# Optimization experiments

Hardware: AMD Instinct MI355X
Metric: run time of the kernel (lower is better)

## Reference

```python
import jax, jax.numpy as jnp
import numpy as np

CLS_W = 1.0
REG_W = 1.0
POS_THR = 0.6
THR_LOW = 0.3
THR_HIGH = 0.6
N_POS = 16
N_NEG = 48
BATCH = 4096
NUM_ANCHOR = 5
FS = 17
SEARCH = 255


def make_anchors():
    # SiamRPN-style anchors: 5 aspect ratios, base size 64, stride 8, 17x17 grid
    ratios = np.array([0.33, 0.5, 1.0, 2.0, 3.0], dtype=np.float64)
    size, stride = 64.0, 8
    ws = np.sqrt(size * size / ratios)            # (K,)
    hs = ws * ratios                              # (K,)
    c = (np.arange(FS) - FS // 2) * stride + SEARCH // 2  # grid centers
    cx = np.broadcast_to(c[None, None, :], (NUM_ANCHOR, FS, FS))
    cy = np.broadcast_to(c[None, :, None], (NUM_ANCHOR, FS, FS))
    w = np.broadcast_to(ws[:, None, None], (NUM_ANCHOR, FS, FS))
    h = np.broadcast_to(hs[:, None, None], (NUM_ANCHOR, FS, FS))
    center = np.stack([cx, cy, w, h], 0).reshape(4, -1).T               # (A,4) cx,cy,w,h
    corner = np.stack([cx - w / 2, cy - h / 2, cx + w / 2, cy + h / 2], 0).reshape(4, -1).T
    return center.astype(np.float32), corner.astype(np.float32)


def setup_inputs() -> dict:
    key = jax.random.key(0)
    k1, k2, k3, k4 = jax.random.split(key, 4)
    pred_cls = jax.random.normal(k1, (BATCH, NUM_ANCHOR, FS, FS), dtype=jnp.float32)
    pred_reg = jax.random.normal(k2, (BATCH, 4, NUM_ANCHOR, FS, FS), dtype=jnp.float32)
    # valid GT boxes inside the search region, overlapping anchor sizes
    cxy = jax.random.uniform(k3, (BATCH, 2), minval=90.0, maxval=165.0)
    wh = jax.random.uniform(k4, (BATCH, 2), minval=35.0, maxval=110.0)
    gt_bbox = jnp.concatenate([cxy - wh / 2, cxy + wh / 2], axis=1).astype(jnp.float32)
    center, corner = make_anchors()
    return {
        "pred_cls": pred_cls,
        "pred_reg": pred_reg,
        "gt_bbox": gt_bbox,
        "anchor_center": jnp.asarray(center),
        "anchor_corner": jnp.asarray(corner),
    }


def jaccard(box_a, box_b):
    # box_a (N,4), box_b (A,4) in x1,y1,x2,y2 -> (N,A) IoU
    lt = jnp.maximum(box_a[:, None, :2], box_b[None, :, :2])
    rb = jnp.minimum(box_a[:, None, 2:], box_b[None, :, 2:])
    wh = jnp.clip(rb - lt, 0.0)
    inter = wh[..., 0] * wh[..., 1]
    area_a = (box_a[:, 2] - box_a[:, 0]) * (box_a[:, 3] - box_a[:, 1])
    area_b = (box_b[:, 2] - box_b[:, 0]) * (box_b[:, 3] - box_b[:, 1])
    return inter / (area_a[:, None] + area_b[None, :] - inter)


def _rand_rank(k, m, A):
    # rank of each index among masked entries under a random shuffle
    u = jax.random.uniform(k, (A,))
    s = jnp.where(m, u, jnp.inf)
    order = jnp.argsort(s)
    return jnp.zeros((A,), jnp.int32).at[order].set(jnp.arange(A, dtype=jnp.int32))


def _forward(pred_cls, pred_reg, gt_bbox, anchor_center, anchor_corner):
    N = pred_cls.shape[0]
    A = anchor_center.shape[0]
    iou = jaccard(gt_bbox, anchor_corner)                       # (N,A)
    matched = jnp.where(iou > THR_HIGH, 1.0, jnp.where(iou < THR_LOW, 0.0, -1.0))
    ks = jax.random.split(jax.random.key(42), 2 * N)
    kpos, kneg = ks[:N], ks[N:]

    def per_sample(cls, reg, gt, mask, kp, kn):
        clsf = cls.reshape(-1)                                  # (A,)
        regf = reg.reshape(4, -1).T                             # (A,4)
        pos = mask == 1.0
        neg = mask == 0.0
        n_pos = jnp.sum(pos).astype(jnp.int32)
        n_neg = jnp.sum(neg).astype(jnp.int32)
        rp = _rand_rank(kp, pos, A)
        rn = _rand_rank(kn, neg, A)
        k_p = jnp.minimum(n_pos, N_POS)                         # sampled positives
        k_n_cap = jnp.where(n_pos > 0, 3 * n_pos, N_NEG)        # int(n_pos*48/16) = 3*n_pos
        k_n = jnp.minimum(n_neg, k_n_cap)
        sel_p = pos & (rp < k_p)
        sel_n = neg & (rn < k_n)
        bce_p = jnp.logaddexp(0.0, -clsf)                       # BCEWithLogits, target 1
        bce_n = jnp.logaddexp(0.0, clsf)                        # BCEWithLogits, target 0
        denom = jnp.maximum(k_p + k_n, 1).astype(clsf.dtype)
        loss_cls_i = (jnp.sum(bce_p * sel_p) + jnp.sum(bce_n * sel_n)) / denom
        acc_i = (jnp.sum((clsf >= POS_THR) & pos) + jnp.sum((clsf < POS_THR) & (~pos))).astype(clsf.dtype) / A
        gcx = (gt[0] + gt[2]) * 0.5
        gcy = (gt[1] + gt[3]) * 0.5
        gw = gt[2] - gt[0]
        gh = gt[3] - gt[1]
        acx, acy, aw, ah = anchor_center[:, 0], anchor_center[:, 1], anchor_center[:, 2], anchor_center[:, 3]
        tgt = jnp.stack([(gcx - acx) / aw, (gcy - acy) / ah, jnp.log(gw / aw), jnp.log(gh / ah)], axis=1)
        np_safe = jnp.maximum(n_pos, 1).astype(clsf.dtype)
        loss_reg_i = jnp.where(n_pos > 0,
                               jnp.sum(((regf - tgt) ** 2) * pos[:, None]) / (4.0 * np_safe),
                               0.0)
        return loss_cls_i, loss_reg_i, acc_i

    lc, lr, ac = jax.vmap(per_sample)(pred_cls, pred_reg, gt_bbox, matched, kpos, kneg)
    loss_cls = jnp.mean(lc)
    loss_reg = jnp.mean(lr)
    acc_cls = jnp.mean(ac)
    loss_total = CLS_W * loss_cls + REG_W * loss_reg
    return loss_total, loss_cls, loss_reg, acc_cls


def reference(pred_cls, pred_reg, gt_bbox, anchor_center, anchor_corner):
    return _forward(pred_cls, pred_reg, gt_bbox, anchor_center, anchor_corner)
```

## Files before the change

### kernel.cpp

```cpp
#include <hip/hip_runtime.h>
#include <stdint.h>
#include <math.h>


#define A_TOT 1445
#define NITER 23
#define WPB 4
#define POS_MAX 64
#define CAND_MAX 128

__device__ __forceinline__ void tf2x32(uint32_t k0, uint32_t k1, uint32_t x0, uint32_t x1,
                                       uint32_t& o0, uint32_t& o1)
{
  const uint32_t k2 = k0 ^ k1 ^ 0x1BD11BDAu;
  x0 += k0; x1 += k1;
#define TFR(r) { x0 += x1; x1 = __builtin_rotateleft32(x1, (r)); x1 ^= x0; }
  TFR(13) TFR(15) TFR(26) TFR(6)
  x0 += k1; x1 += k2 + 1u;
  TFR(17) TFR(29) TFR(16) TFR(24)
  x0 += k2; x1 += k0 + 2u;
  TFR(13) TFR(15) TFR(26) TFR(6)
  x0 += k0; x1 += k1 + 3u;
  TFR(17) TFR(29) TFR(16) TFR(24)
  x0 += k1; x1 += k2 + 4u;
  TFR(13) TFR(15) TFR(26) TFR(6)
  x0 += k2; x1 += k0 + 5u;
#undef TFR
  o0 = x0; o1 = x1;
}

__device__ __forceinline__ float lae0(float x){
  return fmaxf(x, 0.0f) + __logf(1.0f + __expf(-fabsf(x)));
}

__global__ void __attribute__((amdgpu_waves_per_eu(4, 4)))
__launch_bounds__(WPB * 64) rpn_loss_kernel(
    const float* __restrict__ pred_cls, const float* __restrict__ pred_reg,
    const float* __restrict__ gt_bbox, const float* __restrict__ anchor_center,
    const float* __restrict__ anchor_corner,
    float* __restrict__ part,
    int N)
{
  __shared__ uint32_t s_rnm[WPB][A_TOT];
  __shared__ uint32_t s_hist[WPB][256];
  __shared__ uint32_t s_pidx[WPB][POS_MAX];
  __shared__ float    s_pcls[WPB][POS_MAX];
  __shared__ uint32_t s_cand[WPB][CAND_MAX];

  const int w    = threadIdx.x >> 6;
  const int lane = threadIdx.x & 63;
  const int n    = blockIdx.x * WPB + w;
  const uint64_t lmask_lt = (1ull << lane) - 1ull;

  #pragma unroll
  for (int b = 0; b < 4; b++) s_hist[w][lane * 4 + b] = 0u;

  const float g0 = gt_bbox[4 * n + 0];
  const float g1 = gt_bbox[4 * n + 1];
  const float g2 = gt_bbox[4 * n + 2];
  const float g3 = gt_bbox[4 * n + 3];
  const float area_a = (g2 - g0) * (g3 - g1);

  uint32_t kp0, kp1, kn0, kn1;
  tf2x32(0u, 42u, 0u, (uint32_t)n,       kp0, kp1);
  tf2x32(0u, 42u, 0u, (uint32_t)(N + n), kn0, kn1);

  const float*  cls_base = pred_cls + (size_t)n * A_TOT;
  const float4* cornv = (const float4*)anchor_corner;

  uint32_t posCnt = 0u, negCnt = 0u;
  float accc = 0.0f;

  #pragma unroll
  for (int t = 0; t < NITER; t++){
    int j = lane + 64 * t;
    bool valid = (j < A_TOT);
    int jc = valid ? j : (A_TOT - 1);
    float4 cr = cornv[jc];
    float c = cls_base[jc];
    float ltx = fmaxf(g0, cr.x), lty = fmaxf(g1, cr.y);
    float rbx = fminf(g2, cr.z), rby = fminf(g3, cr.w);
    float inter = fmaxf(rbx - ltx, 0.0f) * fmaxf(rby - lty, 0.0f);
    float area_b = (cr.z - cr.x) * (cr.w - cr.y);
    float iou = inter / (area_a + area_b - inter);
    bool pos = valid && (iou > 0.6f);
    bool neg = valid && (iou < 0.3f);
    uint32_t o0, o1;
    tf2x32(kn0, kn1, 0u, (uint32_t)j, o0, o1);
    uint32_t r = (o0 ^ o1) >> 9;
    uint32_t enc = pos ? 2u : (neg ? 0u : 1u);
    if (valid) s_rnm[w][j] = (r << 2) | enc;
    if (neg)   atomicAdd(&s_hist[w][r >> 15], 1u);
    uint64_t pm = __ballot(pos);
    if (pos){
      uint32_t id = posCnt + (uint32_t)__popcll(pm & lmask_lt);
      if (id < POS_MAX){ s_pidx[w][id] = (uint32_t)j; s_pcls[w][id] = c; }
    }
    posCnt += (uint32_t)__popcll(pm);
    negCnt += (uint32_t)__popcll(__ballot(neg));
    accc += (valid && ((c >= 0.6f) == pos)) ? 1.0f : 0.0f;
  }

  const int n_pos = min((int)posCnt, POS_MAX);
  const int n_neg = (int)negCnt;
  const int k_p = min(n_pos, 16);
  const int k_n = min(n_neg, (n_pos > 0) ? 3 * n_pos : 48);

  uint32_t S0, S1, S2, S3;
  {
    int b = lane * 4;
    uint32_t v0 = s_hist[w][b], v1 = s_hist[w][b+1], v2 = s_hist[w][b+2], v3 = s_hist[w][b+3];
    S0 = v0; S1 = S0 + v1; S2 = S1 + v2; S3 = S2 + v3;
    uint32_t x = S3;
    #pragma unroll
    for (int off = 1; off < 64; off <<= 1){
      uint32_t tmp = __shfl_up(x, off, 64);
      if (lane >= off) x += tmp;
    }
    uint32_t excl = x - S3;
    S0 += excl; S1 += excl; S2 += excl; S3 += excl;
    s_hist[w][b] = S0; s_hist[w][b+1] = S1; s_hist[w][b+2] = S2; s_hist[w][b+3] = S3;
  }

  int Bb = 256, m = 0;
  if (k_n > 0){
    unsigned long long bal = __ballot(S3 >= (uint32_t)k_n);
    int fl = __ffsll(bal) - 1;
    uint32_t t0 = __shfl(S0, fl, 64), t1 = __shfl(S1, fl, 64), t2 = __shfl(S2, fl, 64);
    int sub = (t0 >= (uint32_t)k_n) ? 0 : ((t1 >= (uint32_t)k_n) ? 1 : ((t2 >= (uint32_t)k_n) ? 2 : 3));
    Bb = fl * 4 + sub;
    uint32_t before = (Bb == 0) ? 0u : s_hist[w][Bb - 1];
    m = k_n - (int)before;
  }

  float lc = 0.0f, lr = 0.0f;
  if (n_pos > 0){
    uint32_t myr = 0u, myj = 0u; float myc = 0.0f;
    if (lane < n_pos){
      myj = s_pidx[w][lane];
      myc = s_pcls[w][lane];
      uint32_t o0, o1;
      tf2x32(kp0, kp1, 0u, myj, o0, o1);
      myr = (o0 ^ o1) >> 9;
    }
    int rank = 0;
    for (int l = 0; l < n_pos; l++){
      uint32_t r2 = __shfl(myr, l, 64), j2 = __shfl(myj, l, 64);
      if (lane < n_pos && (r2 < myr || (r2 == myr && j2 < myj))) rank++;
    }
    if (lane < n_pos){
      if (rank < k_p) lc += lae0(-myc);
      float gcx = (g0 + g2) * 0.5f, gcy = (g1 + g3) * 0.5f;
      float gw = g2 - g0, gh = g3 - g1;
      float4 ce = ((const float4*)anchor_center)[myj];
      const float* reg_base = pred_reg + (size_t)n * 4 * A_TOT;
      float t0 = (gcx - ce.x) / ce.z;
      float t1 = (gcy - ce.y) / ce.w;
      float t2 = __logf(gw / ce.z);
      float t3 = __logf(gh / ce.w);
      float d0 = reg_base[myj]             - t0;
      float d1 = reg_base[A_TOT + myj]     - t1;
      float d2 = reg_base[2 * A_TOT + myj] - t2;
      float d3 = reg_base[3 * A_TOT + myj] - t3;
      lr = d0 * d0 + d1 * d1 + d2 * d2 + d3 * d3;
    }
  }

  if (k_n > 0){
    uint32_t candCnt = 0u;
    #pragma unroll
    for (int t = 0; t < NITER; t++){
      int j = lane + 64 * t;
      bool valid = (j < A_TOT);
      uint32_t word = valid ? s_rnm[w][j] : 1u;
      bool isneg = (word & 3u) == 0u;
      int bin = (int)(word >> 17);
      if (isneg && bin < Bb) lc += lae0(cls_base[j]);
      bool inB = isneg && (bin == Bb);
      uint64_t bm = __ballot(inB);
      if (inB){
        uint32_t id = candCnt + (uint32_t)__popcll(bm & lmask_lt);
        if (id < CAND_MAX)
          s_cand[w][id] = (((word >> 2) & 0x7FFFu) << 11) | (uint32_t)j;
      }
      candCnt += (uint32_t)__popcll(bm);
    }
    const int L = min((int)candCnt, CAND_MAX);
    for (int c2 = lane; c2 < L; c2 += 64){
      uint32_t my = s_cand[w][c2];
      int rank = 0;
      for (int l = 0; l < L; l++) rank += (s_cand[w][l] < my) ? 1 : 0;
      if (rank < m) lc += lae0(cls_base[my & 0x7FFu]);
    }
  }

  float v0 = lc, v1 = lr, v2 = accc;
  #pragma unroll
  for (int off = 32; off > 0; off >>= 1){
    v0 += __shfl_down(v0, off, 64);
    v1 += __shfl_down(v1, off, 64);
    v2 += __shfl_down(v2, off, 64);
  }
  if (lane == 0){
    int denom = k_p + k_n; if (denom < 1) denom = 1;
    part[n]         = v0 / (float)denom;
    part[N + n]     = (n_pos > 0) ? (v1 / (4.0f * (float)n_pos)) : 0.0f;
    part[2 * N + n] = v2 * (1.0f / (float)A_TOT);
  }
}

__global__ void __launch_bounds__(256) reduce_kernel(const float* __restrict__ part,
                                                     float* __restrict__ out, int N)
{
  const int tid = threadIdx.x;
  float lc = 0.0f, lr = 0.0f, ac = 0.0f;
  for (int i = tid; i < N; i += 256){
    lc += part[i];
    lr += part[N + i];
    ac += part[2 * N + i];
  }
  __shared__ float s[12];
  #pragma unroll
  for (int off = 32; off > 0; off >>= 1){
    lc += __shfl_down(lc, off, 64);
    lr += __shfl_down(lr, off, 64);
    ac += __shfl_down(ac, off, 64);
  }
  const int wave = tid >> 6, lane = tid & 63;
  if (lane == 0){ s[wave] = lc; s[4 + wave] = lr; s[8 + wave] = ac; }
  __syncthreads();
  if (tid == 0){
    float LC = s[0] + s[1] + s[2] + s[3];
    float LR = s[4] + s[5] + s[6] + s[7];
    float AC = s[8] + s[9] + s[10] + s[11];
    float inv = 1.0f / (float)N;
    LC *= inv; LR *= inv; AC *= inv;
    out[0] = LC + LR;
    out[1] = LC;
    out[2] = LR;
    out[3] = AC;
  }
}

extern "C" void kernel_launch(void* const* d_in, const int* in_sizes, int n_in,
                              void* d_out, int out_size, void* d_ws, size_t ws_size,
                              hipStream_t stream)
{
  const float* pred_cls = (const float*)d_in[0];
  const float* pred_reg = (const float*)d_in[1];
  const float* gt_bbox  = (const float*)d_in[2];
  const float* a_center = (const float*)d_in[3];
  const float* a_corner = (const float*)d_in[4];
  float* part = (float*)d_ws;
  float* out  = (float*)d_out;

  const int N = in_sizes[2] / 4;

  hipLaunchKernelGGL(rpn_loss_kernel, dim3(N / WPB), dim3(WPB * 64), 0, stream,
                     pred_cls, pred_reg, gt_bbox, a_center, a_corner, part, N);
  hipLaunchKernelGGL(reduce_kernel, dim3(1), dim3(256), 0, stream, part, out, N);
}
```

Before: 172.0 us.

## Split each sample across two waves with shared-memory atomics and block syncs

Each sample is now handled by two wavefronts instead of one. The anchor loop is split 12/11 iterations between them, positive and candidate collection use LDS atomics in place of ballot prefix sums, and the histogram scan runs on one wave while the other computes positive ranking and regression. Partial sums are combined through shared memory. This doubles the number of waves for the same work and raises the occupancy hint, aiming to hide latency better, at the cost of several __syncthreads, atomic contention and the loss of deterministic positive ordering.

```diff
diff --git a/kernel.cpp b/kernel.cpp
--- a/kernel.cpp
+++ b/kernel.cpp
@@ -5,7 +5,8 @@
 
 #define A_TOT 1445
 #define NITER 23
-#define WPB 4
+#define SPB 2
+#define BLOCK (SPB * 2 * 64)
 #define POS_MAX 64
 #define CAND_MAX 128
 
@@ -33,27 +34,32 @@
   return fmaxf(x, 0.0f) + __logf(1.0f + __expf(-fabsf(x)));
 }
 
-__global__ void __attribute__((amdgpu_waves_per_eu(4, 4)))
-__launch_bounds__(WPB * 64) rpn_loss_kernel(
+__global__ void __attribute__((amdgpu_waves_per_eu(8)))
+__launch_bounds__(BLOCK) rpn_loss_kernel(
     const float* __restrict__ pred_cls, const float* __restrict__ pred_reg,
     const float* __restrict__ gt_bbox, const float* __restrict__ anchor_center,
     const float* __restrict__ anchor_corner,
     float* __restrict__ part,
     int N)
 {
-  __shared__ uint32_t s_rnm[WPB][A_TOT];
-  __shared__ uint32_t s_hist[WPB][256];
-  __shared__ uint32_t s_pidx[WPB][POS_MAX];
-  __shared__ float    s_pcls[WPB][POS_MAX];
-  __shared__ uint32_t s_cand[WPB][CAND_MAX];
-
-  const int w    = threadIdx.x >> 6;
-  const int lane = threadIdx.x & 63;
-  const int n    = blockIdx.x * WPB + w;
-  const uint64_t lmask_lt = (1ull << lane) - 1ull;
-
-  #pragma unroll
-  for (int b = 0; b < 4; b++) s_hist[w][lane * 4 + b] = 0u;
+  __shared__ uint32_t s_rnm[SPB][A_TOT];
+  __shared__ uint32_t s_hist[SPB][256];
+  __shared__ uint32_t s_pidx[SPB][POS_MAX];
+  __shared__ float    s_pcls[SPB][POS_MAX];
+  __shared__ uint32_t s_cand[SPB][CAND_MAX];
+  __shared__ uint32_t s_cnt[SPB][4];
+  __shared__ float    s_red[SPB][2][3];
+
+  const int tid  = threadIdx.x;
+  const int w    = tid >> 6;
+  const int lane = tid & 63;
+  const int s    = w >> 1;
+  const int half = w & 1;
+  const int n    = blockIdx.x * SPB + s;
+
+  s_hist[s][half * 128 + lane * 2 + 0] = 0u;
+  s_hist[s][half * 128 + lane * 2 + 1] = 0u;
+  if (half == 0 && lane < 4) s_cnt[s][lane] = 0u;
 
   const float g0 = gt_bbox[4 * n + 0];
   const float g1 = gt_bbox[4 * n + 1];
@@ -61,18 +67,17 @@
   const float g3 = gt_bbox[4 * n + 3];
   const float area_a = (g2 - g0) * (g3 - g1);
 
-  uint32_t kp0, kp1, kn0, kn1;
-  tf2x32(0u, 42u, 0u, (uint32_t)n,       kp0, kp1);
+  uint32_t kn0, kn1;
   tf2x32(0u, 42u, 0u, (uint32_t)(N + n), kn0, kn1);
 
   const float*  cls_base = pred_cls + (size_t)n * A_TOT;
   const float4* cornv = (const float4*)anchor_corner;
 
-  uint32_t posCnt = 0u, negCnt = 0u;
+  __syncthreads();
+
   float accc = 0.0f;
-
-  #pragma unroll
-  for (int t = 0; t < NITER; t++){
+  const int t0 = half * 12, t1 = half ? NITER : 12;
+  for (int t = t0; t < t1; t++){
     int j = lane + 64 * t;
     bool valid = (j < A_TOT);
     int jc = valid ? j : (A_TOT - 1);
@@ -89,28 +94,24 @@
     tf2x32(kn0, kn1, 0u, (uint32_t)j, o0, o1);
     uint32_t r = (o0 ^ o1) >> 9;
     uint32_t enc = pos ? 2u : (neg ? 0u : 1u);
-    if (valid) s_rnm[w][j] = (r << 2) | enc;
-    if (neg)   atomicAdd(&s_hist[w][r >> 15], 1u);
-    uint64_t pm = __ballot(pos);
+    if (valid) s_rnm[s][j] = (r << 2) | enc;
+    if (neg)   atomicAdd(&s_hist[s][r >> 15], 1u);
     if (pos){
-      uint32_t id = posCnt + (uint32_t)__popcll(pm & lmask_lt);
-      if (id < POS_MAX){ s_pidx[w][id] = (uint32_t)j; s_pcls[w][id] = c; }
-    }
-    posCnt += (uint32_t)__popcll(pm);
-    negCnt += (uint32_t)__popcll(__ballot(neg));
+      uint32_t id = atomicAdd(&s_cnt[s][0], 1u);
+      if (id < POS_MAX){ s_pidx[s][id] = (uint32_t)j; s_pcls[s][id] = c; }
+    }
     accc += (valid && ((c >= 0.6f) == pos)) ? 1.0f : 0.0f;
   }
-
-  const int n_pos = min((int)posCnt, POS_MAX);
-  const int n_neg = (int)negCnt;
+  __syncthreads();
+
+  const int n_pos = (int)s_cnt[s][0];
   const int k_p = min(n_pos, 16);
-  const int k_n = min(n_neg, (n_pos > 0) ? 3 * n_pos : 48);
-
-  uint32_t S0, S1, S2, S3;
-  {
+
+  float lc = 0.0f, lr = 0.0f;
+  if (half == 0){
     int b = lane * 4;
-    uint32_t v0 = s_hist[w][b], v1 = s_hist[w][b+1], v2 = s_hist[w][b+2], v3 = s_hist[w][b+3];
-    S0 = v0; S1 = S0 + v1; S2 = S1 + v2; S3 = S2 + v3;
+    uint32_t v0 = s_hist[s][b], v1 = s_hist[s][b+1], v2 = s_hist[s][b+2], v3 = s_hist[s][b+3];
+    uint32_t S0 = v0, S1 = S0 + v1, S2 = S1 + v2, S3 = S2 + v3;
     uint32_t x = S3;
     #pragma unroll
     for (int off = 1; off < 64; off <<= 1){
@@ -119,77 +120,91 @@
     }
     uint32_t excl = x - S3;
     S0 += excl; S1 += excl; S2 += excl; S3 += excl;
-    s_hist[w][b] = S0; s_hist[w][b+1] = S1; s_hist[w][b+2] = S2; s_hist[w][b+3] = S3;
-  }
-
-  int Bb = 256, m = 0;
+    s_hist[s][b] = S3;
+    const int n_neg = (int)__shfl(S3, 63, 64);
+    const int k_n = min(n_neg, (n_pos > 0) ? 3 * n_pos : 48);
+    int Bb = 256, m = 0;
+    if (k_n > 0){
+      unsigned long long bal = __ballot(S3 >= (uint32_t)k_n);
+      int fl = __ffsll(bal) - 1;
+      uint32_t u0 = __shfl(S0, fl, 64), u1 = __shfl(S1, fl, 64), u2 = __shfl(S2, fl, 64);
+      int sub = (u0 >= (uint32_t)k_n) ? 0 : ((u1 >= (uint32_t)k_n) ? 1 : ((u2 >= (uint32_t)k_n) ? 2 : 3));
+      Bb = fl * 4 + sub;
+      uint32_t before;
+      if (sub == 0) before = (fl == 0) ? 0u : __shfl(S3, fl - 1, 64);
+      else          before = (sub == 1) ? u0 : ((sub == 2) ? u1 : u2);
+      m = k_n - (int)before;
+    }
+    if (lane == 0){
+      s_cnt[s][2] = ((uint32_t)Bb << 16) | (uint32_t)m;
+      s_cnt[s][3] = (uint32_t)n_neg;
+    }
+  } else {
+    if (n_pos > 0){
+      uint32_t kp0, kp1;
+      tf2x32(0u, 42u, 0u, (uint32_t)n, kp0, kp1);
+      uint32_t myr = 0u, myj = 0u; float myc = 0.0f;
+      int npc = min(n_pos, POS_MAX);
+      if (lane < npc){
+        myj = s_pidx[s][lane];
+        myc = s_pcls[s][lane];
+        uint32_t o0, o1;
+        tf2x32(kp0, kp1, 0u, myj, o0, o1);
+        myr = (o0 ^ o1) >> 9;
+      }
+      int rank = 0;
+      for (int l = 0; l < npc; l++){
+        uint32_t r2 = __shfl(myr, l, 64), j2 = __shfl(myj, l, 64);
+        if (lane < npc && (r2 < myr || (r2 == myr && j2 < myj))) rank++;
+      }
+      if (lane < npc){
+        if (rank < k_p) lc += lae0(-myc);
+        float gcx = (g0 + g2) * 0.5f, gcy = (g1 + g3) * 0.5f;
+        float gw = g2 - g0, gh = g3 - g1;
+        float4 ce = ((const float4*)anchor_center)[myj];
+        const float* reg_base = pred_reg + (size_t)n * 4 * A_TOT;
+        float q0 = (gcx - ce.x) / ce.z;
+        float q1 = (gcy - ce.y) / ce.w;
+        float q2 = __logf(gw / ce.z);
+        float q3 = __logf(gh / ce.w);
+        float d0 = reg_base[myj]             - q0;
+        float d1 = reg_base[A_TOT + myj]     - q1;
+        float d2 = reg_base[2 * A_TOT + myj] - q2;
+        float d3 = reg_base[3 * A_TOT + myj] - q3;
+        lr = d0 * d0 + d1 * d1 + d2 * d2 + d3 * d3;
+      }
+    }
+  }
+  __syncthreads();
+
+  const int n_neg = (int)s_cnt[s][3];
+  const int k_n = min(n_neg, (n_pos > 0) ? 3 * n_pos : 48);
+  const uint32_t bm = s_cnt[s][2];
+  const int Bb = (int)(bm >> 16), m = (int)(bm & 0xFFFFu);
+
   if (k_n > 0){
-    unsigned long long bal = __ballot(S3 >= (uint32_t)k_n);
-    int fl = __ffsll(bal) - 1;
-    uint32_t t0 = __shfl(S0, fl, 64), t1 = __shfl(S1, fl, 64), t2 = __shfl(S2, fl, 64);
-    int sub = (t0 >= (uint32_t)k_n) ? 0 : ((t1 >= (uint32_t)k_n) ? 1 : ((t2 >= (uint32_t)k_n) ? 2 : 3));
-    Bb = fl * 4 + sub;
-    uint32_t before = (Bb == 0) ? 0u : s_hist[w][Bb - 1];
-    m = k_n - (int)before;
-  }
-
-  float lc = 0.0f, lr = 0.0f;
-  if (n_pos > 0){
-    uint32_t myr = 0u, myj = 0u; float myc = 0.0f;
-    if (lane < n_pos){
-      myj = s_pidx[w][lane];
-      myc = s_pcls[w][lane];
-      uint32_t o0, o1;
-      tf2x32(kp0, kp1, 0u, myj, o0, o1);
-      myr = (o0 ^ o1) >> 9;
-    }
-    int rank = 0;
-    for (int l = 0; l < n_pos; l++){
-      uint32_t r2 = __shfl(myr, l, 64), j2 = __shfl(myj, l, 64);
-      if (lane < n_pos && (r2 < myr || (r2 == myr && j2 < myj))) rank++;
-    }
-    if (lane < n_pos){
-      if (rank < k_p) lc += lae0(-myc);
-      float gcx = (g0 + g2) * 0.5f, gcy = (g1 + g3) * 0.5f;
-      float gw = g2 - g0, gh = g3 - g1;
-      float4 ce = ((const float4*)anchor_center)[myj];
-      const float* reg_base = pred_reg + (size_t)n * 4 * A_TOT;
-      float t0 = (gcx - ce.x) / ce.z;
-      float t1 = (gcy - ce.y) / ce.w;
-      float t2 = __logf(gw / ce.z);
-      float t3 = __logf(gh / ce.w);
-      float d0 = reg_base[myj]             - t0;
-      float d1 = reg_base[A_TOT + myj]     - t1;
-      float d2 = reg_base[2 * A_TOT + myj] - t2;
-      float d3 = reg_base[3 * A_TOT + myj] - t3;
-      lr = d0 * d0 + d1 * d1 + d2 * d2 + d3 * d3;
-    }
-  }
-
-  if (k_n > 0){
-    uint32_t candCnt = 0u;
-    #pragma unroll
-    for (int t = 0; t < NITER; t++){
+    for (int t = t0; t < t1; t++){
       int j = lane + 64 * t;
       bool valid = (j < A_TOT);
-      uint32_t word = valid ? s_rnm[w][j] : 1u;
+      uint32_t word = valid ? s_rnm[s][j] : 1u;
       bool isneg = (word & 3u) == 0u;
       int bin = (int)(word >> 17);
       if (isneg && bin < Bb) lc += lae0(cls_base[j]);
-      bool inB = isneg && (bin == Bb);
-      uint64_t bm = __ballot(inB);
-      if (inB){
-        uint32_t id = candCnt + (uint32_t)__popcll(bm & lmask_lt);
+      if (isneg && bin == Bb){
+        uint32_t id = atomicAdd(&s_cnt[s][1], 1u);
         if (id < CAND_MAX)
-          s_cand[w][id] = (((word >> 2) & 0x7FFFu) << 11) | (uint32_t)j;
-      }
-      candCnt += (uint32_t)__popcll(bm);
-    }
-    const int L = min((int)candCnt, CAND_MAX);
+          s_cand[s][id] = (((word >> 2) & 0x7FFFu) << 11) | (uint32_t)j;
+      }
+    }
+  }
+  __syncthreads();
+
+  if (half == 0 && k_n > 0){
+    const int L = min((int)s_cnt[s][1], CAND_MAX);
     for (int c2 = lane; c2 < L; c2 += 64){
-      uint32_t my = s_cand[w][c2];
+      uint32_t my = s_cand[s][c2];
       int rank = 0;
-      for (int l = 0; l < L; l++) rank += (s_cand[w][l] < my) ? 1 : 0;
+      for (int l = 0; l < L; l++) rank += (s_cand[s][l] < my) ? 1 : 0;
       if (rank < m) lc += lae0(cls_base[my & 0x7FFu]);
     }
   }
@@ -202,10 +217,17 @@
     v2 += __shfl_down(v2, off, 64);
   }
   if (lane == 0){
+    s_red[s][half][0] = v0; s_red[s][half][1] = v1; s_red[s][half][2] = v2;
+  }
+  __syncthreads();
+  if (half == 0 && lane == 0){
+    float slc = s_red[s][0][0] + s_red[s][1][0];
+    float slr = s_red[s][0][1] + s_red[s][1][1];
+    float sac = s_red[s][0][2] + s_red[s][1][2];
     int denom = k_p + k_n; if (denom < 1) denom = 1;
-    part[n]         = v0 / (float)denom;
-    part[N + n]     = (n_pos > 0) ? (v1 / (4.0f * (float)n_pos)) : 0.0f;
-    part[2 * N + n] = v2 * (1.0f / (float)A_TOT);
+    part[n]         = slc / (float)denom;
+    part[N + n]     = (n_pos > 0) ? (slr / (4.0f * (float)n_pos)) : 0.0f;
+    part[2 * N + n] = sac * (1.0f / (float)A_TOT);
   }
 }
 
@@ -256,7 +278,7 @@
 
   const int N = in_sizes[2] / 4;
 
-  hipLaunchKernelGGL(rpn_loss_kernel, dim3(N / WPB), dim3(WPB * 64), 0, stream,
+  hipLaunchKernelGGL(rpn_loss_kernel, dim3(N / SPB), dim3(BLOCK), 0, stream,
                      pred_cls, pred_reg, gt_bbox, a_center, a_corner, part, N);
   hipLaunchKernelGGL(reduce_kernel, dim3(1), dim3(256), 0, stream, part, out, N);
 }
```

After: 174.7 us. Within noise of the previous version (+1.6%).
